# Optimization experiments

Hardware: AMD Instinct MI355X
Metric: run time of the kernel (lower is better)

Reference implementation:

```python
import jax, jax.numpy as jnp
import numpy as np

K = 10
SLOPE = 0.2
FEATS = [3, 64, 128, 256, 512, 1024]
MLP = [1024, 128, 64, 1]
B, N = 8, 2048


def setup_inputs() -> dict:
    key = jax.random.key(0)
    keys = jax.random.split(key, 32)
    inp = {"x": jax.random.normal(keys[0], (B, N, 3), dtype=jnp.float32)}
    ki = 1
    for i in range(5):
        fin, fout = 2 * FEATS[i], FEATS[i + 1]
        s = 1.0 / np.sqrt(fin)
        inp[f"w{i}"] = jax.random.uniform(keys[ki], (fin, fout), jnp.float32, -s, s); ki += 1
        inp[f"b{i}"] = jax.random.uniform(keys[ki], (fout,), jnp.float32, -s, s); ki += 1
    for i in range(3):
        fin, fout = MLP[i], MLP[i + 1]
        s = 1.0 / np.sqrt(fin)
        inp[f"m{i}w"] = jax.random.uniform(keys[ki], (fin, fout), jnp.float32, -s, s); ki += 1
        inp[f"m{i}b"] = jax.random.uniform(keys[ki], (fout,), jnp.float32, -s, s); ki += 1
    return inp


def _knn_idx(xb):
    # xb: [N, F]; squared euclidean distances, self included (dist 0)
    sq = jnp.sum(xb * xb, axis=-1)
    d2 = sq[:, None] + sq[None, :] - 2.0 * (xb @ xb.T)
    _, idx = jax.lax.top_k(-d2, K)  # [N, K] nearest (incl. self)
    return idx


def _edge_conv(x, W, b):
    # x: [B, N, F] -> [B, N, Fout]
    fin = x.shape[-1]
    W1, W2 = W[:fin], W[fin:]  # split concat([x_i, x_j - x_i]) @ W
    idx = jax.vmap(_knn_idx)(x)  # [B, N, K]
    x_j = jax.vmap(lambda xb, ib: xb[ib])(x, idx)  # [B, N, K, F]
    h_center = x @ W1 + b  # [B, N, Fout]
    diff = x_j - x[:, :, None, :]
    h = h_center[:, :, None, :] + jnp.einsum('bnkf,fo->bnko', diff, W2)
    h = jnp.where(h > 0, h, SLOPE * h)  # LeakyReLU(0.2)
    return jnp.max(h, axis=2)  # max aggregation over neighbors


def reference(x, w0, b0, w1, b1, w2, b2, w3, b3, w4, b4,
              m0w, m0b, m1w, m1b, m2w, m2b):
    ws = [(w0, b0), (w1, b1), (w2, b2), (w3, b3), (w4, b4)]
    h = x
    for W, b in ws:
        h = _edge_conv(h, W, b)
    g = jnp.max(h, axis=1)  # MaxPool1d(kernel=2048) -> global max over points: [B, 1024]
    g = g @ m0w + m0b
    g = g @ m1w + m1b
    g = g @ m2w + m2b
    return g  # [B, 1]
```

## Files before the change

kernel.cpp:

```cpp
#include <hip/hip_runtime.h>
#include <hip/hip_bf16.h>
#include <math.h>

#define BB 8
#define NN 2048
#define KK 10
#define BN (BB * NN)
#define HC 1024
#define GCH 64

typedef __attribute__((ext_vector_type(8))) short bf16x8;
typedef __attribute__((ext_vector_type(4))) float f32x4;

__device__ inline unsigned short f2bf(float f) {
    unsigned int u = __float_as_uint(f);
    unsigned int r = u + 0x7fffu + ((u >> 16) & 1u);
    return (unsigned short)(r >> 16);
}
__device__ inline float bf2f(unsigned short h) {
    return __uint_as_float((unsigned int)h << 16);
}

__device__ __forceinline__ void async16(const void* g, void* l) {
    __builtin_amdgcn_global_load_lds(
        (const __attribute__((address_space(1))) void*)g,
        (__attribute__((address_space(3))) void*)l, 16, 0, 0);
}

__global__ void xsplit3_kernel(const float* __restrict__ x,
                               unsigned short* __restrict__ hi,
                               unsigned short* __restrict__ lo,
                               float* __restrict__ sq) {
    int row = blockIdx.x * blockDim.x + threadIdx.x;
    if (row >= BN) return;
    unsigned short hbuf[32], lbuf[32];
#pragma unroll
    for (int f = 0; f < 32; ++f) { hbuf[f] = 0; lbuf[f] = 0; }
    float s = 0.f;
#pragma unroll
    for (int f = 0; f < 3; ++f) {
        float v = x[(size_t)row * 3 + f];
        s += v * v;
        unsigned short h = f2bf(v);
        hbuf[f] = h;
        lbuf[f] = f2bf(v - bf2f(h));
    }
    sq[row] = s;
#pragma unroll
    for (int f = 0; f < 32; f += 8) {
        *(uint4*)&hi[(size_t)row * 32 + f] = *(uint4*)&hbuf[f];
        *(uint4*)&lo[(size_t)row * 32 + f] = *(uint4*)&lbuf[f];
    }
}

__global__ void wsplit_all_kernel(const float* __restrict__ w0, const float* __restrict__ w1,
                                  const float* __restrict__ w2, const float* __restrict__ w3,
                                  const float* __restrict__ w4, unsigned short* __restrict__ WTall) {
    const int fins[5]  = {3, 64, 128, 256, 512};
    const int fpads[5] = {32, 64, 128, 256, 512};
    const int fouts[5] = {64, 128, 256, 512, 1024};
    const int eoff[6]  = {0, 4096, 20480, 86016, 348160, 1396736};
    const int woff[5]  = {0, 8192, 40960, 172032, 696320};
    int i = blockIdx.x * blockDim.x + threadIdx.x;
    if (i >= 1396736) return;
    int l;
    if (i < eoff[1]) l = 0; else if (i < eoff[2]) l = 1;
    else if (i < eoff[3]) l = 2; else if (i < eoff[4]) l = 3; else l = 4;
    int e = i - eoff[l];
    const float* w = (l == 0) ? w0 : (l == 1) ? w1 : (l == 2) ? w2 : (l == 3) ? w3 : w4;
    int fin = fins[l], fpad = fpads[l], fout = fouts[l];
    unsigned short* WT = WTall + woff[l];
    int op = e % (2 * fout);
    int f = e / (2 * fout);
    float v = 0.f;
    if (f < fin) {
        if (op < fout) v = w[(size_t)f * fout + op] - w[(size_t)(fin + f) * fout + op];
        else v = w[(size_t)(fin + f) * fout + (op - fout)];
    }
    unsigned short h = f2bf(v);
    unsigned short lo = f2bf(v - bf2f(h));
    WT[(size_t)op * (2 * fpad) + f] = h;
    WT[(size_t)op * (2 * fpad) + fpad + f] = lo;
}

__global__ __launch_bounds__(256) void knn_gram_kernel(
        const unsigned short* __restrict__ xh, const unsigned short* __restrict__ xl,
        const float* __restrict__ sq, float* __restrict__ d2a,
        float* __restrict__ d2b, int F) {
    int b = blockIdx.y;
    int t = blockIdx.x, ti = 0;
    while (t >= 16 - ti) { t -= 16 - ti; ti++; }
    int tj = ti + t;
    int row0 = ti * 128;
    int col0 = tj * 128;
    const unsigned short* xhb = xh + (size_t)b * NN * F;
    const unsigned short* xlb = xl + (size_t)b * NN * F;
    const float* sqb = sq + (size_t)b * NN;

    __shared__ __align__(16) unsigned char smem_raw[33024];
    unsigned short* Ah = (unsigned short*)smem_raw;
    unsigned short* Al = Ah + 128 * 32;
    unsigned short* Bh = Al + 128 * 32;
    unsigned short* Bl = Bh + 128 * 32;
    float* LT = (float*)smem_raw;

    int tid = threadIdx.x;
    int lane = tid & 63;
    int wave = tid >> 6;
    int wr = (wave >> 1) * 64, wc = (wave & 1) * 64;
    int l15 = lane & 15, kq = lane >> 4;
    int rsub = lane >> 2;
    int csub = (((lane & 3) ^ ((lane >> 3) & 3))) * 8;
    int kqs = (kq ^ ((l15 >> 1) & 3)) * 8;

    f32x4 acc[4][4];
#pragma unroll
    for (int mt = 0; mt < 4; ++mt)
#pragma unroll
        for (int nt = 0; nt < 4; ++nt) acc[mt][nt] = (f32x4){0.f, 0.f, 0.f, 0.f};

    for (int kc = 0; kc < F; kc += 32) {
        __syncthreads();
#pragma unroll
        for (int j = 0; j < 2; ++j) {
            int row = wave * 32 + j * 16 + rsub;
            int dsto = wave * 1024 + j * 512;
            async16(xhb + (size_t)(row0 + row) * F + kc + csub, Ah + dsto);
            async16(xlb + (size_t)(row0 + row) * F + kc + csub, Al + dsto);
            async16(xhb + (size_t)(col0 + row) * F + kc + csub, Bh + dsto);
            async16(xlb + (size_t)(col0 + row) * F + kc + csub, Bl + dsto);
        }
        __syncthreads();
        bf16x8 bh[4], bl[4];
#pragma unroll
        for (int t4 = 0; t4 < 4; ++t4) {
            bh[t4] = *(const bf16x8*)&Bh[(wc + t4 * 16 + l15) * 32 + kqs];
            bl[t4] = *(const bf16x8*)&Bl[(wc + t4 * 16 + l15) * 32 + kqs];
        }
#pragma unroll
        for (int mt = 0; mt < 4; ++mt) {
            bf16x8 ah = *(const bf16x8*)&Ah[(wr + mt * 16 + l15) * 32 + kqs];
            bf16x8 al = *(const bf16x8*)&Al[(wr + mt * 16 + l15) * 32 + kqs];
#pragma unroll
            for (int nt = 0; nt < 4; ++nt) {
                acc[mt][nt] = __builtin_amdgcn_mfma_f32_16x16x32_bf16(ah, bh[nt], acc[mt][nt], 0, 0, 0);
                acc[mt][nt] = __builtin_amdgcn_mfma_f32_16x16x32_bf16(al, bh[nt], acc[mt][nt], 0, 0, 0);
                acc[mt][nt] = __builtin_amdgcn_mfma_f32_16x16x32_bf16(ah, bl[nt], acc[mt][nt], 0, 0, 0);
            }
        }
    }
    {
        float* dst = (col0 < HC) ? d2a : d2b;
        int lc0 = col0 & (HC - 1);
#pragma unroll
        for (int mt = 0; mt < 4; ++mt) {
            int rbase = row0 + wr + mt * 16 + kq * 4;
#pragma unroll
            for (int nt = 0; nt < 4; ++nt) {
                int cc = wc + nt * 16 + l15;
                float sqc = sqb[col0 + cc];
#pragma unroll
                for (int r = 0; r < 4; ++r) {
                    float v = (sqb[rbase + r] + sqc) - 2.f * acc[mt][nt][r];
                    acc[mt][nt][r] = v;
                    dst[((size_t)b * NN + rbase + r) * HC + lc0 + cc] = v;
                }
            }
        }
    }
    if (ti != tj) {
        float* mdst = (row0 < HC) ? d2a : d2b;
        int mc0 = row0 & (HC - 1);
#pragma unroll
        for (int h = 0; h < 2; ++h) {
            __syncthreads();
            if ((wave & 1) == h) {
#pragma unroll
                for (int mt = 0; mt < 4; ++mt)
#pragma unroll
                    for (int nt = 0; nt < 4; ++nt)
#pragma unroll
                        for (int r = 0; r < 4; ++r)
                            LT[(nt * 16 + l15) * 129 + (wr + mt * 16 + kq * 4 + r)] =
                                acc[mt][nt][r];
            }
            __syncthreads();
#pragma unroll
            for (int it = 0; it < 8; ++it) {
                int v = tid + it * 256;
                int lr = v >> 5, c4 = v & 31;
                float4 val;
                val.x = LT[lr * 129 + c4 * 4];
                val.y = LT[lr * 129 + c4 * 4 + 1];
                val.z = LT[lr * 129 + c4 * 4 + 2];
                val.w = LT[lr * 129 + c4 * 4 + 3];
                *(float4*)&mdst[((size_t)b * NN + col0 + h * 64 + lr) * HC + mc0 + c4 * 4] = val;
            }
        }
    }
}

__global__ __launch_bounds__(256) void knn_select_kernel(
        const float* __restrict__ d2a, const float* __restrict__ d2b,
        int* __restrict__ idx) {
    int row = blockIdx.x * 4 + (threadIdx.x >> 6);
    int lane = threadIdx.x & 63;
    const float* ra = d2a + (size_t)row * HC;
    const float* rb = d2b + (size_t)row * HC;

    float4 v[8];
#pragma unroll
    for (int it = 0; it < 4; ++it) {
        v[it]     = *(const float4*)&ra[it * 256 + lane * 4];
        v[it + 4] = *(const float4*)&rb[it * 256 + lane * 4];
    }

    float bestd[KK];
    int besti[KK];
#pragma unroll
    for (int k = 0; k < KK; ++k) { bestd[k] = INFINITY; besti[k] = 0x7fffffff; }

#pragma unroll
    for (int it = 0; it < 8; ++it) {
        int cbase = ((it < 4) ? (it * 256) : (HC + (it - 4) * 256)) + lane * 4;
        float dv[4] = {v[it].x, v[it].y, v[it].z, v[it].w};
#pragma unroll
        for (int s4 = 0; s4 < 4; ++s4) {
            float d = dv[s4];
            if (d < bestd[KK - 1]) {
                bestd[KK - 1] = d;
                besti[KK - 1] = cbase + s4;
#pragma unroll
                for (int s = KK - 1; s > 0; --s) {
                    if (bestd[s] < bestd[s - 1]) {
                        float td = bestd[s]; bestd[s] = bestd[s - 1]; bestd[s - 1] = td;
                        int ti = besti[s]; besti[s] = besti[s - 1]; besti[s - 1] = ti;
                    }
                }
            }
        }
    }

    int h = 0;
    int mywin = 0;
    for (int s = 0; s < KK; ++s) {
        float dd = (h < KK) ? bestd[h] : INFINITY;
        int ii = (h < KK) ? besti[h] : 0x7fffffff;
        float d0 = dd; int i0 = ii;
#pragma unroll
        for (int off = 32; off > 0; off >>= 1) {
            float od = __shfl_xor(dd, off);
            int oi = __shfl_xor(ii, off);
            if (od < dd || (od == dd && oi < ii)) { dd = od; ii = oi; }
        }
        if (lane == s) mywin = ii;
        if (h < KK && i0 == ii && d0 == dd) h++;
    }
    if (lane < KK) idx[(size_t)row * KK + lane] = mywin;
}

__global__ __launch_bounds__(256) void gemm2_mfma_kernel(
        const unsigned short* __restrict__ XSh, const unsigned short* __restrict__ XSl,
        const unsigned short* __restrict__ WT, const float* __restrict__ bias,
        float* __restrict__ Aout, float* __restrict__ Tout, int fin, int fout) {
    int m0 = blockIdx.x * 128;
    int n0 = blockIdx.y * 128;
    __shared__ __align__(16) unsigned short AsB[4 * 128 * 32];
    unsigned short* Ah = AsB;
    unsigned short* Al = Ah + 128 * 32;
    unsigned short* Bh = Al + 128 * 32;
    unsigned short* Bl = Bh + 128 * 32;

    int tid = threadIdx.x;
    int lane = tid & 63;
    int wave = tid >> 6;
    int wr = (wave >> 1) * 64, wc = (wave & 1) * 64;
    int l15 = lane & 15, kq = lane >> 4;
    int rsub = lane >> 2;
    int csub = (((lane & 3) ^ ((lane >> 3) & 3))) * 8;
    int kqs = (kq ^ ((l15 >> 1) & 3)) * 8;
    int w2f = 2 * fin;

    f32x4 acc[4][4];
#pragma unroll
    for (int mt = 0; mt < 4; ++mt)
#pragma unroll
        for (int nt = 0; nt < 4; ++nt) acc[mt][nt] = (f32x4){0.f, 0.f, 0.f, 0.f};

    for (int kc = 0; kc < fin; kc += 32) {
        __syncthreads();
#pragma unroll
        for (int j = 0; j < 2; ++j) {
            int row = wave * 32 + j * 16 + rsub;
            int dsto = wave * 1024 + j * 512;
            async16(XSh + (size_t)(m0 + row) * fin + kc + csub, Ah + dsto);
            async16(XSl + (size_t)(m0 + row) * fin + kc + csub, Al + dsto);
            async16(WT + (size_t)(n0 + row) * w2f + kc + csub, Bh + dsto);
            async16(WT + (size_t)(n0 + row) * w2f + fin + kc + csub, Bl + dsto);
        }
        __syncthreads();
        bf16x8 bh[4], bl[4];
#pragma unroll
        for (int t = 0; t < 4; ++t) {
            bh[t] = *(const bf16x8*)&Bh[(wc + t * 16 + l15) * 32 + kqs];
            bl[t] = *(const bf16x8*)&Bl[(wc + t * 16 + l15) * 32 + kqs];
        }
#pragma unroll
        for (int mt = 0; mt < 4; ++mt) {
            bf16x8 ah = *(const bf16x8*)&Ah[(wr + mt * 16 + l15) * 32 + kqs];
            bf16x8 al = *(const bf16x8*)&Al[(wr + mt * 16 + l15) * 32 + kqs];
#pragma unroll
            for (int nt = 0; nt < 4; ++nt) {
                acc[mt][nt] = __builtin_amdgcn_mfma_f32_16x16x32_bf16(ah, bh[nt], acc[mt][nt], 0, 0, 0);
                acc[mt][nt] = __builtin_amdgcn_mfma_f32_16x16x32_bf16(al, bh[nt], acc[mt][nt], 0, 0, 0);
                acc[mt][nt] = __builtin_amdgcn_mfma_f32_16x16x32_bf16(ah, bl[nt], acc[mt][nt], 0, 0, 0);
            }
        }
    }
#pragma unroll
    for (int mt = 0; mt < 4; ++mt) {
        int mbase = m0 + wr + mt * 16 + kq * 4;
#pragma unroll
        for (int nt = 0; nt < 4; ++nt) {
            int oc = n0 + wc + nt * 16 + l15;
            f32x4 c = acc[mt][nt];
            if (oc < fout) {
                float bv = bias[oc];
#pragma unroll
                for (int r = 0; r < 4; ++r)
                    Aout[(size_t)(mbase + r) * fout + oc] = c[r] + bv;
            } else {
                int o2 = oc - fout;
#pragma unroll
                for (int r = 0; r < 4; ++r)
                    Tout[(size_t)(mbase + r) * fout + o2] = c[r];
            }
        }
    }
}

__device__ __forceinline__ const unsigned short* tbaseA(
        const unsigned short* XSh, const unsigned short* XSl, int F, int t) {
    int ko = t * 64;
    if (ko < F) return XSh + ko;
    if (ko < 2 * F) return XSl + (ko - F);
    return XSh + (ko - 2 * F);
}
__device__ __forceinline__ const unsigned short* tbaseB(
        const unsigned short* WT, int F, int t) {
    int ko = t * 64;
    if (ko < F) return WT + ko;
    if (ko < 2 * F) return WT + (ko - F);
    return WT + F + (ko - 2 * F);
}

#define GBAR() asm volatile("s_barrier" ::: "memory")

__global__ __launch_bounds__(512, 2) void gemm2_8ph_kernel(
        const unsigned short* __restrict__ XSh, const unsigned short* __restrict__ XSl,
        const unsigned short* __restrict__ WT, const float* __restrict__ bias,
        float* __restrict__ Aout, float* __restrict__ Tout, int F, int fout, int nby) {
    __shared__ __align__(16) unsigned short Lds[65536];

    int nwg = gridDim.x;
    int bid = blockIdx.x;
    int q = nwg >> 3;
    int swz = (bid & 7) * q + (bid >> 3);
    int by = swz % nby;
    int bx = swz / nby;
    int m0 = bx * 256, n0 = by * 256;

    int tid = threadIdx.x;
    int lane = tid & 63;
    int wave = tid >> 6;
    int mw = wave >> 2;
    int nw = wave & 3;
    int l15 = lane & 15, kq = lane >> 4;
    int rx7 = l15 & 7;

    int isA = (wave < 4);
    size_t rowmul = isA ? (size_t)F : (size_t)(2 * F);
    int orgn = isA ? m0 : n0;
    int r8 = lane >> 3;
    int cb8 = ((lane & 7) ^ r8) * 8;
    int subb = (wave & 3) * 8;
    int ldsoA = isA ? 0 : 16384;

    int nt = (3 * F) >> 6;

    f32x4 acc[8][4];
#pragma unroll
    for (int mt = 0; mt < 8; ++mt)
#pragma unroll
        for (int nn = 0; nn < 4; ++nn) acc[mt][nn] = (f32x4){0.f, 0.f, 0.f, 0.f};

    auto stage = [&](const unsigned short* tb, int par, int j) {
        int sub = subb + j;
        async16(tb + (size_t)(orgn + sub * 8 + r8) * rowmul + cb8,
                Lds + par * 32768 + ldsoA + sub * 512);
    };

    {
        const unsigned short* t0 = isA ? tbaseA(XSh, XSl, F, 0) : tbaseB(WT, F, 0);
        const unsigned short* t1 = isA ? tbaseA(XSh, XSl, F, 1) : tbaseB(WT, F, 1);
#pragma unroll
        for (int j = 0; j < 8; ++j) stage(t0, 0, j);
#pragma unroll
        for (int j = 0; j < 4; ++j) stage(t1, 1, j);
    }
    asm volatile("s_waitcnt vmcnt(4)" ::: "memory");
    GBAR();

    for (int t = 0; t < nt; ++t) {
        const unsigned short* Ab = Lds + (t & 1) * 32768;
        const unsigned short* Bb = Ab + 16384;
        bool s1 = (t + 1 < nt), s2 = (t + 2 < nt);
        const unsigned short* tb1 = s1 ? (isA ? tbaseA(XSh, XSl, F, t + 1)
                                              : tbaseB(WT, F, t + 1)) : XSh;
        const unsigned short* tb2 = s2 ? (isA ? tbaseA(XSh, XSl, F, t + 2)
                                              : tbaseB(WT, F, t + 2)) : XSh;
        int p1 = (t + 1) & 1, p0 = t & 1;

        bf16x8 aF[4][2], bA[2][2], bB[2][2];

#pragma unroll
        for (int mt = 0; mt < 4; ++mt)
#pragma unroll
            for (int kf = 0; kf < 2; ++kf)
                aF[mt][kf] = *(const bf16x8*)&Ab[(mw * 128 + mt * 16 + l15) * 64 +
                                                 ((kf * 4 + kq) ^ rx7) * 8];
#pragma unroll
        for (int nn = 0; nn < 2; ++nn)
#pragma unroll
            for (int kf = 0; kf < 2; ++kf)
                bA[nn][kf] = *(const bf16x8*)&Bb[(nw * 64 + nn * 16 + l15) * 64 +
                                                 ((kf * 4 + kq) ^ rx7) * 8];
        if (s1) { stage(tb1, p1, 4); stage(tb1, p1, 5); }
        GBAR();
        __builtin_amdgcn_s_setprio(1);
#pragma unroll
        for (int mt = 0; mt < 4; ++mt)
#pragma unroll
            for (int nn = 0; nn < 2; ++nn) {
                acc[mt][nn] = __builtin_amdgcn_mfma_f32_16x16x32_bf16(aF[mt][0], bA[nn][0], acc[mt][nn], 0, 0, 0);
                acc[mt][nn] = __builtin_amdgcn_mfma_f32_16x16x32_bf16(aF[mt][1], bA[nn][1], acc[mt][nn], 0, 0, 0);
            }
        __builtin_amdgcn_s_setprio(0);
        GBAR();

#pragma unroll
        for (int nn = 0; nn < 2; ++nn)
#pragma unroll
            for (int kf = 0; kf < 2; ++kf)
                bB[nn][kf] = *(const bf16x8*)&Bb[(nw * 64 + (nn + 2) * 16 + l15) * 64 +
                                                 ((kf * 4 + kq) ^ rx7) * 8];
        if (s1) { stage(tb1, p1, 6); stage(tb1, p1, 7); }
        GBAR();
        __builtin_amdgcn_s_setprio(1);
#pragma unroll
        for (int mt = 0; mt < 4; ++mt)
#pragma unroll
            for (int nn = 0; nn < 2; ++nn) {
                acc[mt][nn + 2] = __builtin_amdgcn_mfma_f32_16x16x32_bf16(aF[mt][0], bB[nn][0], acc[mt][nn + 2], 0, 0, 0);
                acc[mt][nn + 2] = __builtin_amdgcn_mfma_f32_16x16x32_bf16(aF[mt][1], bB[nn][1], acc[mt][nn + 2], 0, 0, 0);
            }
        __builtin_amdgcn_s_setprio(0);
        GBAR();

#pragma unroll
        for (int mt = 0; mt < 4; ++mt)
#pragma unroll
            for (int kf = 0; kf < 2; ++kf)
                aF[mt][kf] = *(const bf16x8*)&Ab[(mw * 128 + (mt + 4) * 16 + l15) * 64 +
                                                 ((kf * 4 + kq) ^ rx7) * 8];
        GBAR();
        __builtin_amdgcn_s_setprio(1);
#pragma unroll
        for (int mt = 0; mt < 4; ++mt)
#pragma unroll
            for (int nn = 0; nn < 2; ++nn) {
                acc[mt + 4][nn] = __builtin_amdgcn_mfma_f32_16x16x32_bf16(aF[mt][0], bA[nn][0], acc[mt + 4][nn], 0, 0, 0);
                acc[mt + 4][nn] = __builtin_amdgcn_mfma_f32_16x16x32_bf16(aF[mt][1], bA[nn][1], acc[mt + 4][nn], 0, 0, 0);
            }
        __builtin_amdgcn_s_setprio(0);
        GBAR();

        if (s2) { stage(tb2, p0, 0); stage(tb2, p0, 1); stage(tb2, p0, 2); stage(tb2, p0, 3); }
        GBAR();
        __builtin_amdgcn_s_setprio(1);
#pragma unroll
        for (int mt = 0; mt < 4; ++mt)
#pragma unroll
            for (int nn = 0; nn < 2; ++nn) {
                acc[mt + 4][nn + 2] = __builtin_amdgcn_mfma_f32_16x16x32_bf16(aF[mt][0], bB[nn][0], acc[mt + 4][nn + 2], 0, 0, 0);
                acc[mt + 4][nn + 2] = __builtin_amdgcn_mfma_f32_16x16x32_bf16(aF[mt][1], bB[nn][1], acc[mt + 4][nn + 2], 0, 0, 0);
            }
        __builtin_amdgcn_s_setprio(0);
        if (s2)      asm volatile("s_waitcnt vmcnt(4)" ::: "memory");
        else if (s1) asm volatile("s_waitcnt vmcnt(0)" ::: "memory");
        GBAR();
    }

#pragma unroll
    for (int mt = 0; mt < 8; ++mt) {
        int mbase = m0 + mw * 128 + mt * 16 + kq * 4;
#pragma unroll
        for (int nn = 0; nn < 4; ++nn) {
            int oc = n0 + nw * 64 + nn * 16 + l15;
            f32x4 c = acc[mt][nn];
            if (oc < fout) {
                float bv = bias[oc];
#pragma unroll
                for (int r = 0; r < 4; ++r)
                    Aout[(size_t)(mbase + r) * fout + oc] = c[r] + bv;
            } else {
                int o2 = oc - fout;
#pragma unroll
                for (int r = 0; r < 4; ++r)
                    Tout[(size_t)(mbase + r) * fout + o2] = c[r];
            }
        }
    }
}

__global__ __launch_bounds__(256) void gathermax_fused_kernel(
        const float* __restrict__ A, const float* __restrict__ T,
        const int* __restrict__ idx, unsigned short* __restrict__ hi,
        unsigned short* __restrict__ lo, float* __restrict__ sq, int shift) {
    int b = blockIdx.y;
    int wave = threadIdx.x >> 6;
    int lane = threadIdx.x & 63;
    int pnl = blockIdx.x * 4 + wave;
    int pn = (b << 11) + pnl;
    int fout = 1 << shift;
    int nf4 = fout >> 2;
    const float* Tb = T + ((size_t)b << 11) * fout;
    const int* ip = idx + (size_t)pn * KK;
    int j[KK];
#pragma unroll
    for (int k = 0; k < KK; ++k) j[k] = ip[k];

    float s = 0.f;
    for (int f4 = lane; f4 < nf4; f4 += 64) {
        int o = f4 * 4;
        float4 m = {-INFINITY, -INFINITY, -INFINITY, -INFINITY};
#pragma unroll
        for (int k = 0; k < KK; ++k) {
            float4 t = *(const float4*)&Tb[(size_t)j[k] * fout + o];
            m.x = fmaxf(m.x, t.x); m.y = fmaxf(m.y, t.y);
            m.z = fmaxf(m.z, t.z); m.w = fmaxf(m.w, t.w);
        }
        float4 a = *(const float4*)&A[(size_t)pn * fout + o];
        float h4[4];
        h4[0] = a.x + m.x; h4[1] = a.y + m.y; h4[2] = a.z + m.z; h4[3] = a.w + m.w;
        uint2 uh, ul;
        unsigned short hs[4], ls[4];
#pragma unroll
        for (int q = 0; q < 4; ++q) {
            float h = h4[q] > 0.f ? h4[q] : 0.2f * h4[q];
            s += h * h;
            unsigned short hh = f2bf(h);
            hs[q] = hh;
            ls[q] = f2bf(h - bf2f(hh));
        }
        uh.x = (unsigned)hs[0] | ((unsigned)hs[1] << 16);
        uh.y = (unsigned)hs[2] | ((unsigned)hs[3] << 16);
        ul.x = (unsigned)ls[0] | ((unsigned)ls[1] << 16);
        ul.y = (unsigned)ls[2] | ((unsigned)ls[3] << 16);
        *(uint2*)&hi[(size_t)pn * fout + o] = uh;
        *(uint2*)&lo[(size_t)pn * fout + o] = ul;
    }
#pragma unroll
    for (int off = 32; off > 0; off >>= 1) s += __shfl_down(s, off);
    if (lane == 0) sq[pn] = s;
}

__global__ __launch_bounds__(256) void gathermax_gmax_kernel(
        const float* __restrict__ A, const float* __restrict__ T,
        const int* __restrict__ idx, float* __restrict__ gp) {
    int chunk = blockIdx.x;
    int b = blockIdx.y;
    int o = threadIdx.x * 4;
    const float* Tb = T + ((size_t)b << 11) * 1024;
    float4 gm = {-INFINITY, -INFINITY, -INFINITY, -INFINITY};
    for (int p = 0; p < NN / GCH; ++p) {
        int pnl = chunk * (NN / GCH) + p;
        int pn = (b << 11) + pnl;
        const int* ip = idx + (size_t)pn * KK;
        float4 m = {-INFINITY, -INFINITY, -INFINITY, -INFINITY};
#pragma unroll
        for (int k = 0; k < KK; ++k) {
            int j = ip[k];
            float4 t = *(const float4*)&Tb[(size_t)j * 1024 + o];
            m.x = fmaxf(m.x, t.x); m.y = fmaxf(m.y, t.y);
            m.z = fmaxf(m.z, t.z); m.w = fmaxf(m.w, t.w);
        }
        float4 a = *(const float4*)&A[(size_t)pn * 1024 + o];
        float4 h;
        h.x = a.x + m.x; h.y = a.y + m.y; h.z = a.z + m.z; h.w = a.w + m.w;
        h.x = h.x > 0.f ? h.x : 0.2f * h.x;
        h.y = h.y > 0.f ? h.y : 0.2f * h.y;
        h.z = h.z > 0.f ? h.z : 0.2f * h.z;
        h.w = h.w > 0.f ? h.w : 0.2f * h.w;
        gm.x = fmaxf(gm.x, h.x); gm.y = fmaxf(gm.y, h.y);
        gm.z = fmaxf(gm.z, h.z); gm.w = fmaxf(gm.w, h.w);
    }
    *(float4*)&gp[((size_t)chunk * BB + b) * 1024 + o] = gm;
}

__global__ void gmax2_kernel(const float* __restrict__ gp, float* __restrict__ g) {
    int i = blockIdx.x * 256 + threadIdx.x;
    int b = i >> 10, o = i & 1023;
    float m = -INFINITY;
    for (int c = 0; c < GCH; ++c) m = fmaxf(m, gp[((size_t)c * BB + b) * 1024 + o]);
    g[(size_t)b * 1024 + o] = m;
}

__global__ __launch_bounds__(256) void mlp1_kernel(
        const float* __restrict__ g, const float* __restrict__ m0w,
        const float* __restrict__ m0b, float* __restrict__ H1) {
    int wid = blockIdx.x * 4 + (threadIdx.x >> 6);
    int lane = threadIdx.x & 63;
    int b = wid >> 7, t = wid & 127;
    float s = 0.f;
    for (int f = lane; f < 1024; f += 64)
        s += g[(size_t)b * 1024 + f] * m0w[(size_t)f * 128 + t];
#pragma unroll
    for (int off = 32; off > 0; off >>= 1) s += __shfl_down(s, off);
    if (lane == 0) H1[(size_t)b * 128 + t] = s + m0b[t];
}

__global__ __launch_bounds__(256) void mlp2_kernel(
        const float* __restrict__ H1, const float* __restrict__ m1w,
        const float* __restrict__ m1b, float* __restrict__ H2) {
    int wid = blockIdx.x * 4 + (threadIdx.x >> 6);
    int lane = threadIdx.x & 63;
    int b = wid >> 6, t = wid & 63;
    float s = 0.f;
    for (int f = lane; f < 128; f += 64)
        s += H1[(size_t)b * 128 + f] * m1w[(size_t)f * 64 + t];
#pragma unroll
    for (int off = 32; off > 0; off >>= 1) s += __shfl_down(s, off);
    if (lane == 0) H2[(size_t)b * 64 + t] = s + m1b[t];
}

__global__ __launch_bounds__(256) void mlp3_kernel(
        const float* __restrict__ H2, const float* __restrict__ m2w,
        const float* __restrict__ m2b, float* __restrict__ out) {
    int b = blockIdx.x * 4 + (threadIdx.x >> 6);
    int lane = threadIdx.x & 63;
    if (b >= BB) return;
    float s = H2[(size_t)b * 64 + lane] * m2w[lane];
#pragma unroll
    for (int off = 32; off > 0; off >>= 1) s += __shfl_down(s, off);
    if (lane == 0) out[b] = s + m2b[0];
}

extern "C" void kernel_launch(void* const* d_in, const int* in_sizes, int n_in,
                              void* d_out, int out_size, void* d_ws, size_t ws_size,
                              hipStream_t stream) {
    const float* x0 = (const float*)d_in[0];
    const float* w[5], * bi[5];
    for (int i = 0; i < 5; ++i) { w[i] = (const float*)d_in[1 + 2 * i]; bi[i] = (const float*)d_in[2 + 2 * i]; }
    const float* m0w = (const float*)d_in[11]; const float* m0b = (const float*)d_in[12];
    const float* m1w = (const float*)d_in[13]; const float* m1b = (const float*)d_in[14];
    const float* m2w = (const float*)d_in[15]; const float* m2b = (const float*)d_in[16];

    const int fouts[5] = {64, 128, 256, 512, 1024};
    const int shifts[5] = {6, 7, 8, 9, 10};
    const int woff[5] = {0, 8192, 40960, 172032, 696320};
    const size_t WTALL = 2793472;

    float* X0 = (float*)d_ws;
    float* X1 = X0 + (size_t)BN * 1024;
    float* T  = X1 + (size_t)BN * 1024;
    float* SQ = T  + (size_t)BN * 1024;
    int*   IDX = (int*)(SQ + BN);
    unsigned short* XSh = (unsigned short*)(IDX + (size_t)BN * KK);
    unsigned short* XSl = XSh + (size_t)BN * 512;
    unsigned short* WTall = XSl + (size_t)BN * 512;
    float* GP = (float*)(WTall + WTALL);
    float* G  = GP + (size_t)GCH * BB * 1024;
    float* H1 = G + (size_t)BB * 1024;
    float* H2 = H1 + (size_t)BB * 128;
    float* bufs[2] = {X0, X1};

    xsplit3_kernel<<<(BN + 255) / 256, 256, 0, stream>>>(x0, XSh, XSl, SQ);
    wsplit_all_kernel<<<(1396736 + 255) / 256, 256, 0, stream>>>(w[0], w[1], w[2], w[3], w[4], WTall);

    int fin = 3;
    for (int l = 0; l < 5; ++l) {
        int fout = fouts[l];
        float* nxt = bufs[l & 1];
        int Fg = (l == 0) ? 32 : fin;

        dim3 gg2(136, BB);
        knn_gram_kernel<<<gg2, 256, 0, stream>>>(XSh, XSl, SQ, T, nxt, Fg);
        knn_select_kernel<<<BN / 4, 256, 0, stream>>>(T, nxt, IDX);

        if (l >= 2) {
            int nby = (2 * fout) / 256;
            gemm2_8ph_kernel<<<dim3(64 * nby), 512, 0, stream>>>(
                XSh, XSl, WTall + woff[l], bi[l], nxt, T, fin, fout, nby);
        } else {
            dim3 gg(BN / 128, (2 * fout) / 128);
            gemm2_mfma_kernel<<<gg, 256, 0, stream>>>(XSh, XSl, WTall + woff[l], bi[l], nxt, T, Fg, fout);
        }

        if (l < 4) {
            dim3 gmg(NN / 4, BB);
            gathermax_fused_kernel<<<gmg, 256, 0, stream>>>(nxt, T, IDX, XSh, XSl, SQ, shifts[l]);
        } else {
            dim3 gmg(GCH, BB);
            gathermax_gmax_kernel<<<gmg, 256, 0, stream>>>(nxt, T, IDX, GP);
        }

        fin = fout;
    }

    gmax2_kernel<<<32, 256, 0, stream>>>(GP, G);
    mlp1_kernel<<<256, 256, 0, stream>>>(G, m0w, m0b, H1);
    mlp2_kernel<<<128, 256, 0, stream>>>(H1, m1w, m1b, H2);
    mlp3_kernel<<<2, 256, 0, stream>>>(H2, m2w, m2b, (float*)d_out);
}
```

Baseline: 1.002 ms.

## Software-pipeline LDS fragment loads across GEMM k-iterations with fewer barriers

Restructures the GEMM main loop so that A/B register fragments for the next k-tile are read from LDS while the last MFMA block of the current tile runs. Barriers between fragment reads and MFMA blocks are removed, going from eight per iteration to roughly four. This targets LDS-read latency and barrier stalls in the edge-conv GEMM, at the cost of more live registers (separate a03/a47/b01/b23 fragments) and tighter correctness reasoning about LDS buffer reuse.

```diff
diff --git a/kernel.cpp b/kernel.cpp
--- a/kernel.cpp
+++ b/kernel.cpp
@@ -399,6 +399,14 @@
         async16(tb + (size_t)(orgn + sub * 8 + r8) * rowmul + cb8,
                 Lds + par * 32768 + ldsoA + sub * 512);
     };
+    auto rdA = [&](const unsigned short* Ab, int mt, int kf) -> bf16x8 {
+        return *(const bf16x8*)&Ab[(mw * 128 + mt * 16 + l15) * 64 +
+                                   ((kf * 4 + kq) ^ rx7) * 8];
+    };
+    auto rdB = [&](const unsigned short* Bb, int nn, int kf) -> bf16x8 {
+        return *(const bf16x8*)&Bb[(nw * 64 + nn * 16 + l15) * 64 +
+                                   ((kf * 4 + kq) ^ rx7) * 8];
+    };
 
     {
         const unsigned short* t0 = isA ? tbaseA(XSh, XSl, F, 0) : tbaseB(WT, F, 0);
@@ -411,94 +419,96 @@
     asm volatile("s_waitcnt vmcnt(4)" ::: "memory");
     GBAR();
 
+    bf16x8 a03[4][2], a47[4][2], b01[2][2], b23[2][2];
+#pragma unroll
+    for (int mt = 0; mt < 4; ++mt)
+#pragma unroll
+        for (int kf = 0; kf < 2; ++kf) a03[mt][kf] = rdA(Lds, mt, kf);
+#pragma unroll
+    for (int nn = 0; nn < 2; ++nn)
+#pragma unroll
+        for (int kf = 0; kf < 2; ++kf) b01[nn][kf] = rdB(Lds + 16384, nn, kf);
+
     for (int t = 0; t < nt; ++t) {
         const unsigned short* Ab = Lds + (t & 1) * 32768;
         const unsigned short* Bb = Ab + 16384;
+        const unsigned short* An = Lds + ((t + 1) & 1) * 32768;
+        const unsigned short* Bn = An + 16384;
         bool s1 = (t + 1 < nt), s2 = (t + 2 < nt);
         const unsigned short* tb1 = s1 ? (isA ? tbaseA(XSh, XSl, F, t + 1)
                                               : tbaseB(WT, F, t + 1)) : XSh;
-        const unsigned short* tb2 = s2 ? (isA ? tbaseA(XSh, XSl, F, t + 2)
-                                              : tbaseB(WT, F, t + 2)) : XSh;
         int p1 = (t + 1) & 1, p0 = t & 1;
 
-        bf16x8 aF[4][2], bA[2][2], bB[2][2];
-
+#pragma unroll
+        for (int nn = 0; nn < 2; ++nn)
+#pragma unroll
+            for (int kf = 0; kf < 2; ++kf) b23[nn][kf] = rdB(Bb, nn + 2, kf);
+        if (s1) { stage(tb1, p1, 4); stage(tb1, p1, 5); }
+        __builtin_amdgcn_s_setprio(1);
 #pragma unroll
         for (int mt = 0; mt < 4; ++mt)
 #pragma unroll
-            for (int kf = 0; kf < 2; ++kf)
-                aF[mt][kf] = *(const bf16x8*)&Ab[(mw * 128 + mt * 16 + l15) * 64 +
-                                                 ((kf * 4 + kq) ^ rx7) * 8];
-#pragma unroll
-        for (int nn = 0; nn < 2; ++nn)
-#pragma unroll
-            for (int kf = 0; kf < 2; ++kf)
-                bA[nn][kf] = *(const bf16x8*)&Bb[(nw * 64 + nn * 16 + l15) * 64 +
-                                                 ((kf * 4 + kq) ^ rx7) * 8];
-        if (s1) { stage(tb1, p1, 4); stage(tb1, p1, 5); }
-        GBAR();
-        __builtin_amdgcn_s_setprio(1);
-#pragma unroll
-        for (int mt = 0; mt < 4; ++mt)
-#pragma unroll
             for (int nn = 0; nn < 2; ++nn) {
-                acc[mt][nn] = __builtin_amdgcn_mfma_f32_16x16x32_bf16(aF[mt][0], bA[nn][0], acc[mt][nn], 0, 0, 0);
-                acc[mt][nn] = __builtin_amdgcn_mfma_f32_16x16x32_bf16(aF[mt][1], bA[nn][1], acc[mt][nn], 0, 0, 0);
+                acc[mt][nn] = __builtin_amdgcn_mfma_f32_16x16x32_bf16(a03[mt][0], b01[nn][0], acc[mt][nn], 0, 0, 0);
+                acc[mt][nn] = __builtin_amdgcn_mfma_f32_16x16x32_bf16(a03[mt][1], b01[nn][1], acc[mt][nn], 0, 0, 0);
             }
         __builtin_amdgcn_s_setprio(0);
         GBAR();
 
 #pragma unroll
-        for (int nn = 0; nn < 2; ++nn)
-#pragma unroll
-            for (int kf = 0; kf < 2; ++kf)
-                bB[nn][kf] = *(const bf16x8*)&Bb[(nw * 64 + (nn + 2) * 16 + l15) * 64 +
-                                                 ((kf * 4 + kq) ^ rx7) * 8];
+        for (int mt = 0; mt < 4; ++mt)
+#pragma unroll
+            for (int kf = 0; kf < 2; ++kf) a47[mt][kf] = rdA(Ab, mt + 4, kf);
         if (s1) { stage(tb1, p1, 6); stage(tb1, p1, 7); }
-        GBAR();
         __builtin_amdgcn_s_setprio(1);
 #pragma unroll
         for (int mt = 0; mt < 4; ++mt)
 #pragma unroll
             for (int nn = 0; nn < 2; ++nn) {
-                acc[mt][nn + 2] = __builtin_amdgcn_mfma_f32_16x16x32_bf16(aF[mt][0], bB[nn][0], acc[mt][nn + 2], 0, 0, 0);
-                acc[mt][nn + 2] = __builtin_amdgcn_mfma_f32_16x16x32_bf16(aF[mt][1], bB[nn][1], acc[mt][nn + 2], 0, 0, 0);
+                acc[mt][nn + 2] = __builtin_amdgcn_mfma_f32_16x16x32_bf16(a03[mt][0], b23[nn][0], acc[mt][nn + 2], 0, 0, 0);
+                acc[mt][nn + 2] = __builtin_amdgcn_mfma_f32_16x16x32_bf16(a03[mt][1], b23[nn][1], acc[mt][nn + 2], 0, 0, 0);
             }
         __builtin_amdgcn_s_setprio(0);
         GBAR();
 
+        __builtin_amdgcn_s_setprio(1);
 #pragma unroll
         for (int mt = 0; mt < 4; ++mt)
 #pragma unroll
-            for (int kf = 0; kf < 2; ++kf)
-                aF[mt][kf] = *(const bf16x8*)&Ab[(mw * 128 + (mt + 4) * 16 + l15) * 64 +
-                                                 ((kf * 4 + kq) ^ rx7) * 8];
-        GBAR();
-        __builtin_amdgcn_s_setprio(1);
-#pragma unroll
-        for (int mt = 0; mt < 4; ++mt)
-#pragma unroll
             for (int nn = 0; nn < 2; ++nn) {
-                acc[mt + 4][nn] = __builtin_amdgcn_mfma_f32_16x16x32_bf16(aF[mt][0], bA[nn][0], acc[mt + 4][nn], 0, 0, 0);
-                acc[mt + 4][nn] = __builtin_amdgcn_mfma_f32_16x16x32_bf16(aF[mt][1], bA[nn][1], acc[mt + 4][nn], 0, 0, 0);
+                acc[mt + 4][nn] = __builtin_amdgcn_mfma_f32_16x16x32_bf16(a47[mt][0], b01[nn][0], acc[mt + 4][nn], 0, 0, 0);
+                acc[mt + 4][nn] = __builtin_amdgcn_mfma_f32_16x16x32_bf16(a47[mt][1], b01[nn][1], acc[mt + 4][nn], 0, 0, 0);
             }
         __builtin_amdgcn_s_setprio(0);
         GBAR();
 
-        if (s2) { stage(tb2, p0, 0); stage(tb2, p0, 1); stage(tb2, p0, 2); stage(tb2, p0, 3); }
-        GBAR();
-        __builtin_amdgcn_s_setprio(1);
-#pragma unroll
-        for (int mt = 0; mt < 4; ++mt)
-#pragma unroll
-            for (int nn = 0; nn < 2; ++nn) {
-                acc[mt + 4][nn + 2] = __builtin_amdgcn_mfma_f32_16x16x32_bf16(aF[mt][0], bB[nn][0], acc[mt + 4][nn + 2], 0, 0, 0);
-                acc[mt + 4][nn + 2] = __builtin_amdgcn_mfma_f32_16x16x32_bf16(aF[mt][1], bB[nn][1], acc[mt + 4][nn + 2], 0, 0, 0);
-            }
-        __builtin_amdgcn_s_setprio(0);
+        if (s2) {
+            const unsigned short* tb2 = isA ? tbaseA(XSh, XSl, F, t + 2)
+                                            : tbaseB(WT, F, t + 2);
+            stage(tb2, p0, 0); stage(tb2, p0, 1); stage(tb2, p0, 2); stage(tb2, p0, 3);
+        }
         if (s2)      asm volatile("s_waitcnt vmcnt(4)" ::: "memory");
         else if (s1) asm volatile("s_waitcnt vmcnt(0)" ::: "memory");
-        GBAR();
+        if (s1) {
+            GBAR();
+#pragma unroll
+            for (int mt = 0; mt < 4; ++mt)
+#pragma unroll
+                for (int kf = 0; kf < 2; ++kf) a03[mt][kf] = rdA(An, mt, kf);
+#pragma unroll
+            for (int nn = 0; nn < 2; ++nn)
+#pragma unroll
+                for (int kf = 0; kf < 2; ++kf) b01[nn][kf] = rdB(Bn, nn, kf);
+        }
+        __builtin_amdgcn_s_setprio(1);
+#pragma unroll
+        for (int mt = 0; mt < 4; ++mt)
+#pragma unroll
+            for (int nn = 0; nn < 2; ++nn) {
+                acc[mt + 4][nn + 2] = __builtin_amdgcn_mfma_f32_16x16x32_bf16(a47[mt][0], b23[nn][0], acc[mt + 4][nn + 2], 0, 0, 0);
+                acc[mt + 4][nn + 2] = __builtin_amdgcn_mfma_f32_16x16x32_bf16(a47[mt][1], b23[nn][1], acc[mt + 4][nn + 2], 0, 0, 0);
+            }
+        __builtin_amdgcn_s_setprio(0);
     }
 
 #pragma unroll
```

Result: slower. 1.027 ms (+2.5%).
